# Kernel optimization log

Hardware: AMD Instinct MI355X
Metric: run time of the kernel (lower is better)

Reference implementation:

```python
import jax, jax.numpy as jnp
import numpy as np

N_NODES = 50000
N_EDGES = 800000
IN_DIM = 256
HEADS = 4
HEAD_DIM = 64  # out_dim // heads
NEG_SLOPE = 0.2  # PyG GATConv default


def setup_inputs() -> dict:
    key = jax.random.key(0)
    k1, k2, k3, k4, k5 = jax.random.split(key, 5)
    x = jax.random.normal(k1, (N_NODES, IN_DIM), dtype=jnp.float32)
    edge_index = jax.random.randint(k2, (2, N_EDGES), 0, N_NODES, dtype=jnp.int64)
    # Glorot-ish scaling
    W = jax.random.normal(k3, (IN_DIM, HEADS * HEAD_DIM), dtype=jnp.float32) * (1.0 / np.sqrt(IN_DIM))
    att_src = jax.random.normal(k4, (HEADS, HEAD_DIM), dtype=jnp.float32) * (1.0 / np.sqrt(HEAD_DIM))
    att_dst = jax.random.normal(k5, (HEADS, HEAD_DIM), dtype=jnp.float32) * (1.0 / np.sqrt(HEAD_DIM))
    bias = jnp.zeros((HEADS * HEAD_DIM,), dtype=jnp.float32)
    return {"x": x, "edge_index": edge_index, "W": W, "att_src": att_src,
            "att_dst": att_dst, "bias": bias}


def reference(x, edge_index, W, att_src, att_dst, bias):
    N = x.shape[0]
    # add self-loops (PyG GATConv default)
    loops = jnp.arange(N, dtype=edge_index.dtype)
    src = jnp.concatenate([edge_index[0], loops])
    dst = jnp.concatenate([edge_index[1], loops])

    h = (x @ W).reshape(N, HEADS, HEAD_DIM)          # [N,H,D]
    a_src = jnp.einsum('nhd,hd->nh', h, att_src)     # [N,H]
    a_dst = jnp.einsum('nhd,hd->nh', h, att_dst)     # [N,H]

    e = a_src[src] + a_dst[dst]                      # [E,H]
    e = jax.nn.leaky_relu(e, NEG_SLOPE)

    # segment softmax over edges sharing a destination node
    m = jax.ops.segment_max(e, dst, num_segments=N)  # [N,H]
    e = jnp.exp(e - m[dst])
    denom = jax.ops.segment_sum(e, dst, num_segments=N)  # [N,H]
    alpha = e / denom[dst]                           # [E,H]

    msg = alpha[:, :, None] * h[src]                 # [E,H,D]
    out = jax.ops.segment_sum(msg, dst, num_segments=N)  # [N,H,D]
    return out.reshape(N, HEADS * HEAD_DIM) + bias
```

## Files before the change

kernel.cpp:

```cpp
#include <hip/hip_runtime.h>
#include <hip/hip_bf16.h>

#define N_NODES 50000
#define N_EDGES 800000
#define IN_DIM 256
#define HEADS 4
#define HEAD_DIM 64
#define OUT_DIM 256
#define NEG_SLOPE 0.2f
#define M_PAD 50048
#define SEG_CAP 64

#define GEMM_BLOCKS 782
#define SCAT_BLOCKS 3125
#define PREP_BLOCKS 260

typedef float floatx4 __attribute__((ext_vector_type(4)));
typedef short shortx8 __attribute__((ext_vector_type(8)));

__global__ __launch_bounds__(256) void prep(const float* __restrict__ W,
                                            ushort* __restrict__ Wt,
                                            int* __restrict__ cnt,
                                            int* __restrict__ csr) {
    int b = blockIdx.x;
    if (b < 64) {
        int t = b * 256 + threadIdx.x;
        int n = t >> 6;
        int k = (t & 63) << 2;
        ushort4 o;
        o.x = __bfloat16_as_ushort(__float2bfloat16(W[(size_t)(k + 0) * OUT_DIM + n]));
        o.y = __bfloat16_as_ushort(__float2bfloat16(W[(size_t)(k + 1) * OUT_DIM + n]));
        o.z = __bfloat16_as_ushort(__float2bfloat16(W[(size_t)(k + 2) * OUT_DIM + n]));
        o.w = __bfloat16_as_ushort(__float2bfloat16(W[(size_t)(k + 3) * OUT_DIM + n]));
        *(ushort4*)&Wt[(size_t)n * IN_DIM + k] = o;
    } else {
        int t = (b - 64) * 256 + threadIdx.x;
        if (t < N_NODES) csr[t << 6] = t;
        if (t < 12500) ((int4*)cnt)[t] = make_int4(1, 1, 1, 1);
    }
}

__global__ __launch_bounds__(256) void scatter_kernel(const int* __restrict__ e_src,
                                                      const int* __restrict__ e_dst,
                                                      int* __restrict__ cnt,
                                                      int* __restrict__ csr) {
    int id = blockIdx.x * 256 + threadIdx.x;
    if (id < N_EDGES) {
        int s = e_src[id];
        int d = e_dst[id];
        int pos = atomicAdd(&cnt[d], 1);
        if (pos < SEG_CAP) csr[(d << 6) + pos] = s;
    }
}

__global__ __launch_bounds__(256) void gemm_kernel(const float* __restrict__ x,
                                                   const ushort* __restrict__ Wt,
                                                   const float* __restrict__ att_src,
                                                   const float* __restrict__ att_dst,
                                                   ushort* __restrict__ h2,
                                                   float* __restrict__ asrc,
                                                   float* __restrict__ adst) {
    __shared__ float A_lds[2][64 * 32];

    const int tid = threadIdx.x;
    const int w = tid >> 6;
    const int lane = tid & 63;
    const int quad = lane >> 4;
    const int l16 = lane & 15;
    const int row0 = blockIdx.x * 64;

    auto stage = [&](int buf, int k0) {
#pragma unroll
        for (int i = 0; i < 2; ++i) {
            int s = i * 256 + tid;
            int row = s >> 3;
            int cg = (s & 7) ^ (row & 7);
            int gr = row0 + row;
            if (gr > N_NODES - 1) gr = N_NODES - 1;
            const float* src = &x[(size_t)gr * IN_DIM + k0 + cg * 4];
            __builtin_amdgcn_global_load_lds(
                (const __attribute__((address_space(1))) unsigned int*)src,
                (__attribute__((address_space(3))) unsigned int*)&A_lds[buf][s * 4],
                16, 0, 0);
        }
    };

    floatx4 acc[4][4] = {};
    const ushort* wtb = Wt + (size_t)(w * 64 + l16) * IN_DIM + quad * 8;

    stage(0, 0);
    __syncthreads();
#pragma unroll 2
    for (int t = 0; t < 8; ++t) {
        int cur = t & 1;
        if (t < 7) stage(cur ^ 1, (t + 1) * 32);
        int k0 = t * 32;
        shortx8 bfr[4], af[4];
#pragma unroll
        for (int c = 0; c < 4; ++c)
            bfr[c] = *(const shortx8*)(wtb + (size_t)c * 16 * IN_DIM + k0);
#pragma unroll
        for (int r = 0; r < 4; ++r) {
            const int row = r * 16 + l16;
            const int sw = row & 7;
            const float* Ab = &A_lds[cur][row * 32];
            float4 f0 = *(const float4*)&Ab[((2 * quad) ^ sw) * 4];
            float4 f1 = *(const float4*)&Ab[((2 * quad + 1) ^ sw) * 4];
            float f[8] = {f0.x, f0.y, f0.z, f0.w, f1.x, f1.y, f1.z, f1.w};
            alignas(16) ushort a8[8];
#pragma unroll
            for (int u = 0; u < 8; ++u)
                a8[u] = __bfloat16_as_ushort(__float2bfloat16(f[u]));
            af[r] = *(const shortx8*)a8;
        }
#pragma unroll
        for (int r = 0; r < 4; ++r)
#pragma unroll
            for (int c = 0; c < 4; ++c)
                acc[r][c] = __builtin_amdgcn_mfma_f32_16x16x32_bf16(bfr[c], af[r],
                                                                    acc[r][c], 0, 0, 0);
        __syncthreads();
    }

    float as_cj[16], ad_cj[16];
#pragma unroll
    for (int c = 0; c < 4; ++c)
#pragma unroll
        for (int j = 0; j < 4; ++j) {
            int col = w * 64 + c * 16 + quad * 4 + j;
            as_cj[c * 4 + j] = att_src[col];
            ad_cj[c * 4 + j] = att_dst[col];
        }
#pragma unroll
    for (int r = 0; r < 4; ++r) {
        float s = 0.f, d = 0.f;
        alignas(16) ushort o16[16];
#pragma unroll
        for (int c = 0; c < 4; ++c)
#pragma unroll
            for (int j = 0; j < 4; ++j) {
                float v = acc[r][c][j];
                s = fmaf(v, as_cj[c * 4 + j], s);
                d = fmaf(v, ad_cj[c * 4 + j], d);
                o16[c * 4 + j] = __bfloat16_as_ushort(__float2bfloat16(v));
            }
        s += __shfl_xor(s, 16);
        s += __shfl_xor(s, 32);
        d += __shfl_xor(d, 16);
        d += __shfl_xor(d, 32);
        int gr = row0 + r * 16 + l16;
        if (quad == 0 && gr < N_NODES) {
            asrc[gr * HEADS + w] = s;
            adst[gr * HEADS + w] = d;
        }
        ushort* hp = h2 + (size_t)gr * OUT_DIM + w * 64 + quad * 16;
        *(uint4*)hp = *(const uint4*)&o16[0];
        *(uint4*)(hp + 8) = *(const uint4*)&o16[8];
    }
}

__global__ __launch_bounds__(256) void aggregate_v8(const uint2* __restrict__ h2,
                                                    const float* __restrict__ a_src,
                                                    const float* __restrict__ a_dst,
                                                    const int* __restrict__ cnt,
                                                    const int* __restrict__ csr,
                                                    const float* __restrict__ bias,
                                                    float* __restrict__ out) {
    int n = blockIdx.x * 4 + (threadIdx.x >> 6);
    if (n >= N_NODES) return;
    int lane = threadIdx.x & 63;
    int h = lane >> 4;
    int col0 = ((lane >> 4) << 6) + ((lane & 3) << 4) + (((lane >> 2) & 3) << 2);
    int beg = n << 6;
    int cn = min(cnt[n], SEG_CAP);
    int nfull = cn >> 3, rem = cn & 7;
    float adv = a_dst[n * HEADS + h];

    float den = 0.f;
    float acc0 = 0.f, acc1 = 0.f, acc2 = 0.f, acc3 = 0.f;
    for (int b = 0; b < nfull; ++b) {
        int i = beg + b * 8;
        int4 sa = *(const int4*)&csr[i];
        int4 sb = *(const int4*)&csr[i + 4];
        int ss[8] = {sa.x, sa.y, sa.z, sa.w, sb.x, sb.y, sb.z, sb.w};
        float asv[8];
        uint2 hv[8];
#pragma unroll
        for (int u = 0; u < 8; ++u) {
            asv[u] = a_src[ss[u] * HEADS + h];
            hv[u] = h2[(size_t)ss[u] * 64 + lane];
        }
#pragma unroll
        for (int u = 0; u < 8; ++u) {
            float e = asv[u] + adv;
            e = fmaxf(e, NEG_SLOPE * e);
            float p = __expf(e);
            den += p;
            acc0 = fmaf(p, __uint_as_float(hv[u].x << 16), acc0);
            acc1 = fmaf(p, __uint_as_float(hv[u].x & 0xffff0000u), acc1);
            acc2 = fmaf(p, __uint_as_float(hv[u].y << 16), acc2);
            acc3 = fmaf(p, __uint_as_float(hv[u].y & 0xffff0000u), acc3);
        }
    }
    if (rem) {
        int i = beg + nfull * 8;
        int4 sa = *(const int4*)&csr[i];
        int4 sb = *(const int4*)&csr[i + 4];
        int ss[8] = {sa.x, sa.y, sa.z, sa.w, sb.x, sb.y, sb.z, sb.w};
        float asv[8];
        uint2 hv[8];
#pragma unroll
        for (int u = 0; u < 8; ++u) {
            int s = (u < rem) ? ss[u] : 0;
            asv[u] = a_src[s * HEADS + h];
            hv[u] = h2[(size_t)s * 64 + lane];
        }
#pragma unroll
        for (int u = 0; u < 8; ++u) {
            float e = asv[u] + adv;
            e = fmaxf(e, NEG_SLOPE * e);
            float p = (u < rem) ? __expf(e) : 0.f;
            den += p;
            acc0 = fmaf(p, __uint_as_float(hv[u].x << 16), acc0);
            acc1 = fmaf(p, __uint_as_float(hv[u].x & 0xffff0000u), acc1);
            acc2 = fmaf(p, __uint_as_float(hv[u].y << 16), acc2);
            acc3 = fmaf(p, __uint_as_float(hv[u].y & 0xffff0000u), acc3);
        }
    }
    float idv = 1.0f / den;
    float4 b = *(const float4*)&bias[col0];
    float4 o = make_float4(acc0 * idv + b.x, acc1 * idv + b.y,
                           acc2 * idv + b.z, acc3 * idv + b.w);
    *(float4*)&out[(size_t)n * OUT_DIM + col0] = o;
}

extern "C" void kernel_launch(void* const* d_in, const int* in_sizes, int n_in,
                              void* d_out, int out_size, void* d_ws, size_t ws_size,
                              hipStream_t stream) {
    const float* x = (const float*)d_in[0];
    const int* ei = (const int*)d_in[1];
    const float* W = (const float*)d_in[2];
    const float* att_src = (const float*)d_in[3];
    const float* att_dst = (const float*)d_in[4];
    const float* bias = (const float*)d_in[5];
    float* out = (float*)d_out;

    const int* e_src = ei;
    const int* e_dst = ei + N_EDGES;

    char* p = (char*)d_ws;
    auto alloc = [&](size_t bytes) {
        void* r = (void*)p;
        p += (bytes + 255) & ~(size_t)255;
        return r;
    };
    ushort* h2   = (ushort*)alloc((size_t)M_PAD * OUT_DIM * 2);
    float* asrc  = (float*)alloc((size_t)N_NODES * HEADS * 4);
    float* adst  = (float*)alloc((size_t)N_NODES * HEADS * 4);
    int* cnt     = (int*)alloc((size_t)N_NODES * 4);
    int* csr     = (int*)alloc((size_t)N_NODES * SEG_CAP * 4);
    ushort* Wt   = (ushort*)alloc((size_t)IN_DIM * OUT_DIM * 2);

    prep<<<PREP_BLOCKS, 256, 0, stream>>>(W, Wt, cnt, csr);
    scatter_kernel<<<SCAT_BLOCKS, 256, 0, stream>>>(e_src, e_dst, cnt, csr);
    gemm_kernel<<<GEMM_BLOCKS, 256, 0, stream>>>(x, Wt, att_src, att_dst, h2, asrc, adst);
    aggregate_v8<<<(N_NODES + 3) / 4, 256, 0, stream>>>((const uint2*)h2, asrc, adst,
                                                        cnt, csr, bias, out);
}
```

Before: 246.8 us.

## Merge scatter into GEMM launch and split aggregation per head across XCDs

```diff
diff --git a/kernel.cpp b/kernel.cpp
--- a/kernel.cpp
+++ b/kernel.cpp
@@ -13,7 +13,10 @@
 
 #define GEMM_BLOCKS 782
 #define SCAT_BLOCKS 3125
+#define MEGA_BLOCKS (GEMM_BLOCKS + SCAT_BLOCKS)
 #define PREP_BLOCKS 260
+#define NODE_GROUPS 3125
+#define AGG_BLOCKS 12504
 
 typedef float floatx4 __attribute__((ext_vector_type(4)));
 typedef short shortx8 __attribute__((ext_vector_type(8)));
@@ -40,27 +43,29 @@
     }
 }
 
-__global__ __launch_bounds__(256) void scatter_kernel(const int* __restrict__ e_src,
-                                                      const int* __restrict__ e_dst,
-                                                      int* __restrict__ cnt,
-                                                      int* __restrict__ csr) {
-    int id = blockIdx.x * 256 + threadIdx.x;
-    if (id < N_EDGES) {
-        int s = e_src[id];
-        int d = e_dst[id];
-        int pos = atomicAdd(&cnt[d], 1);
-        if (pos < SEG_CAP) csr[(d << 6) + pos] = s;
-    }
-}
-
-__global__ __launch_bounds__(256) void gemm_kernel(const float* __restrict__ x,
+__global__ __launch_bounds__(256) void mega_kernel(const float* __restrict__ x,
                                                    const ushort* __restrict__ Wt,
                                                    const float* __restrict__ att_src,
                                                    const float* __restrict__ att_dst,
+                                                   const int* __restrict__ e_src,
+                                                   const int* __restrict__ e_dst,
+                                                   int* __restrict__ cnt,
+                                                   int* __restrict__ csr,
                                                    ushort* __restrict__ h2,
                                                    float* __restrict__ asrc,
                                                    float* __restrict__ adst) {
     __shared__ float A_lds[2][64 * 32];
+
+    if (blockIdx.x >= GEMM_BLOCKS) {
+        int id = (blockIdx.x - GEMM_BLOCKS) * 256 + threadIdx.x;
+        if (id < N_EDGES) {
+            int s = e_src[id];
+            int d = e_dst[id];
+            int pos = atomicAdd(&cnt[d], 1);
+            if (pos < SEG_CAP) csr[(d << 6) + pos] = s;
+        }
+        return;
+    }
 
     const int tid = threadIdx.x;
     const int w = tid >> 6;
@@ -159,22 +164,26 @@
     }
 }
 
-__global__ __launch_bounds__(256) void aggregate_v8(const uint2* __restrict__ h2,
+__global__ __launch_bounds__(256) void aggregate_v9(const uint2* __restrict__ h2,
                                                     const float* __restrict__ a_src,
                                                     const float* __restrict__ a_dst,
                                                     const int* __restrict__ cnt,
                                                     const int* __restrict__ csr,
                                                     const float* __restrict__ bias,
                                                     float* __restrict__ out) {
-    int n = blockIdx.x * 4 + (threadIdx.x >> 6);
-    if (n >= N_NODES) return;
-    int lane = threadIdx.x & 63;
-    int h = lane >> 4;
-    int col0 = ((lane >> 4) << 6) + ((lane & 3) << 4) + (((lane >> 2) & 3) << 2);
+    int bid = blockIdx.x;
+    int xcd = bid & 7;
+    int h = xcd >> 1;
+    int g = ((bid >> 3) << 1) + (xcd & 1);
+    if (g >= NODE_GROUPS) return;
+    int n = (g << 4) + (threadIdx.x >> 4);
+    int l = threadIdx.x & 15;
+    int col0 = (h << 6) + ((l & 3) << 4) + (((l >> 2) & 3) << 2);
+    const uint2* h2h = h2 + (h << 4) + l;
     int beg = n << 6;
     int cn = min(cnt[n], SEG_CAP);
     int nfull = cn >> 3, rem = cn & 7;
-    float adv = a_dst[n * HEADS + h];
+    float adv = a_dst[(n << 2) + h];
 
     float den = 0.f;
     float acc0 = 0.f, acc1 = 0.f, acc2 = 0.f, acc3 = 0.f;
@@ -187,8 +196,8 @@
         uint2 hv[8];
 #pragma unroll
         for (int u = 0; u < 8; ++u) {
-            asv[u] = a_src[ss[u] * HEADS + h];
-            hv[u] = h2[(size_t)ss[u] * 64 + lane];
+            asv[u] = a_src[(ss[u] << 2) + h];
+            hv[u] = h2h[(size_t)ss[u] * 64];
         }
 #pragma unroll
         for (int u = 0; u < 8; ++u) {
@@ -212,8 +221,8 @@
 #pragma unroll
         for (int u = 0; u < 8; ++u) {
             int s = (u < rem) ? ss[u] : 0;
-            asv[u] = a_src[s * HEADS + h];
-            hv[u] = h2[(size_t)s * 64 + lane];
+            asv[u] = a_src[(s << 2) + h];
+            hv[u] = h2h[(size_t)s * 64];
         }
 #pragma unroll
         for (int u = 0; u < 8; ++u) {
@@ -262,8 +271,8 @@
     ushort* Wt   = (ushort*)alloc((size_t)IN_DIM * OUT_DIM * 2);
 
     prep<<<PREP_BLOCKS, 256, 0, stream>>>(W, Wt, cnt, csr);
-    scatter_kernel<<<SCAT_BLOCKS, 256, 0, stream>>>(e_src, e_dst, cnt, csr);
-    gemm_kernel<<<GEMM_BLOCKS, 256, 0, stream>>>(x, Wt, att_src, att_dst, h2, asrc, adst);
-    aggregate_v8<<<(N_NODES + 3) / 4, 256, 0, stream>>>((const uint2*)h2, asrc, adst,
-                                                        cnt, csr, bias, out);
-}
+    mega_kernel<<<MEGA_BLOCKS, 256, 0, stream>>>(x, Wt, att_src, att_dst, e_src, e_dst,
+                                                 cnt, csr, h2, asrc, adst);
+    aggregate_v9<<<AGG_BLOCKS, 256, 0, stream>>>((const uint2*)h2, asrc, adst,
+                                                 cnt, csr, bias, out);
+}
```

After: 231.9 us. 1.06x faster.
